# Kernel optimization log

Hardware: AMD Instinct MI355X
Metric: run time of the kernel (lower is better)

## Reference

```python
import math
import jax, jax.numpy as jnp
import numpy as np

R, C, D, ORDER = 2048, 2048, 64, 3
O = ORDER + 1  # var_size


def setup_inputs() -> dict:
    key = jax.random.key(0)
    k1, k2, k3, k4, k5, k6 = jax.random.split(key, 6)
    return {
        "events": jax.random.randint(k1, (R, C), 0, 2, dtype=jnp.int32),
        "col_times": jax.random.uniform(k2, (C,), dtype=jnp.float32),
        "z_rows": jax.random.normal(k3, (O, R, D), dtype=jnp.float32),
        "z_cols": jax.random.normal(k4, (C, D), dtype=jnp.float32),
        "gamma_rows": jax.random.uniform(k5, (R,), dtype=jnp.float32),
        "gamma_cols": jax.random.uniform(k6, (C,), dtype=jnp.float32),
    }


def reference(events, col_times, z_rows, z_cols, gamma_rows, gamma_cols):
    o = z_rows.shape[0]
    facts = np.array([math.factorial(i) for i in range(o)], dtype=np.float32)
    # Taylor time-basis: coeffs[o, c] = t_c^o / o!   (replaces nested Python loops)
    coeffs = jnp.stack([col_times ** i for i in range(o)]) / facts[:, None]  # (O, C)
    # row positions at each column's time: (R, C, D)
    pos = jnp.einsum('ord,oc->rcd', z_rows, coeffs)
    diff = pos - z_cols[None, :, :]                        # (R, C, D)
    dist = jnp.sqrt(jnp.sum(diff * diff, axis=-1))         # (R, C) pairwise L2
    logit = gamma_rows[:, None] + gamma_cols[None, :] - dist
    # log p where p = 1 - E - (1-2E)*sigmoid(logit):
    #   E==1 -> log sigmoid(logit); E==0 -> log sigmoid(-logit)
    sign = jnp.where(events == 1, 1.0, -1.0).astype(logit.dtype)
    log_lik = jnp.sum(jax.nn.log_sigmoid(sign * logit))
    return -log_lik
```

## Files before the change

### kernel.cpp

```cpp
#include <hip/hip_runtime.h>
#include <hip/hip_bf16.h>
#include <math.h>

#define R_DIM 2048
#define C_DIM 2048
#define D_DIM 64
#define K_TOT 288

typedef __attribute__((ext_vector_type(8))) short short8;
typedef __attribute__((ext_vector_type(4))) float floatx4;

__device__ __forceinline__ ushort f2bf(float f) {
  unsigned u = __float_as_uint(f);
  return (ushort)((u + 0x7FFFu + ((u >> 16) & 1u)) >> 16);
}

__global__ void prep_kernel(const int* __restrict__ events,
                            const float* __restrict__ col_times,
                            const float* __restrict__ z_rows,
                            const float* __restrict__ z_cols,
                            ushort* __restrict__ Ab,
                            ushort* __restrict__ Bb,
                            float* __restrict__ nzc,
                            unsigned char* __restrict__ Wb8,
                            float* __restrict__ out) {
  const int b = blockIdx.x;
  const int t = threadIdx.x;
  const int lane = t & 63;

  if (b == 0 && t == 0) out[0] = 0.0f;

  {
    const int4 e0 = *(const int4*)&events[(size_t)b * C_DIM + t * 8];
    const int4 e1 = *(const int4*)&events[(size_t)b * C_DIM + t * 8 + 4];
    const unsigned byte =
        (unsigned)(e0.x & 1) | ((unsigned)(e0.y & 1) << 1) |
        ((unsigned)(e0.z & 1) << 2) | ((unsigned)(e0.w & 1) << 3) |
        ((unsigned)(e1.x & 1) << 4) | ((unsigned)(e1.y & 1) << 5) |
        ((unsigned)(e1.z & 1) << 6) | ((unsigned)(e1.w & 1) << 7);
    Wb8[(size_t)b * 256 + t] = (unsigned char)byte;
  }

  if (t < 64) {
    float zv[4];
#pragma unroll
    for (int o = 0; o < 4; ++o) {
      zv[o] = z_rows[(size_t)(o * R_DIM + b) * D_DIM + lane];
      Ab[(size_t)b * K_TOT + o * 64 + lane] = f2bf(zv[o]);
    }
    float g00 = zv[0] * zv[0], g01 = zv[0] * zv[1], g02 = zv[0] * zv[2],
          g03 = zv[0] * zv[3], g11 = zv[1] * zv[1], g12 = zv[1] * zv[2],
          g13 = zv[1] * zv[3], g22 = zv[2] * zv[2], g23 = zv[2] * zv[3],
          g33 = zv[3] * zv[3];
#pragma unroll
    for (int off = 32; off > 0; off >>= 1) {
      g00 += __shfl_xor(g00, off); g01 += __shfl_xor(g01, off);
      g02 += __shfl_xor(g02, off); g03 += __shfl_xor(g03, off);
      g11 += __shfl_xor(g11, off); g12 += __shfl_xor(g12, off);
      g13 += __shfl_xor(g13, off); g22 += __shfl_xor(g22, off);
      g23 += __shfl_xor(g23, off); g33 += __shfl_xor(g33, off);
    }
    if (lane == 0) {
      ushort* e = Ab + (size_t)b * K_TOT + 256;
      e[0] = f2bf(g00);  e[1] = f2bf(g01);  e[2] = f2bf(g02);  e[3] = f2bf(g03);
      e[4] = f2bf(g01);  e[5] = f2bf(g11);  e[6] = f2bf(g12);  e[7] = f2bf(g13);
      e[8] = f2bf(g02);  e[9] = f2bf(g12);  e[10] = f2bf(g22); e[11] = f2bf(g23);
      e[12] = f2bf(g03); e[13] = f2bf(g13); e[14] = f2bf(g23); e[15] = f2bf(g33);
    }
    if (lane < 16) Ab[(size_t)b * K_TOT + 272 + lane] = 0;
  } else if (t < 128) {
    const float tt = col_times[b];
    float cf[4];
    cf[0] = 1.0f; cf[1] = tt; cf[2] = tt * tt * 0.5f;
    cf[3] = cf[2] * tt * (1.0f / 3.0f);
    const float zc = z_cols[(size_t)b * D_DIM + lane];
#pragma unroll
    for (int o = 0; o < 4; ++o)
      Bb[(size_t)b * K_TOT + o * 64 + lane] = f2bf(-2.0f * cf[o] * zc);
    float q = zc * zc;
#pragma unroll
    for (int off = 32; off > 0; off >>= 1) q += __shfl_xor(q, off);
    if (lane == 0) {
      nzc[b] = q;
      ushort* e = Bb + (size_t)b * K_TOT + 256;
#pragma unroll
      for (int i = 0; i < 16; ++i) e[i] = f2bf(cf[i >> 2] * cf[i & 3]);
    }
    if (lane < 16) Bb[(size_t)b * K_TOT + 272 + lane] = 0;
  }
}

__launch_bounds__(256, 4)
__global__ void pair_kernel(const float* __restrict__ gamma_rows,
                            const float* __restrict__ gamma_cols,
                            const ushort* __restrict__ Ab,
                            const ushort* __restrict__ Bb,
                            const float* __restrict__ nzc,
                            const unsigned char* __restrict__ Wb8,
                            float* __restrict__ out) {
  __shared__ float red[4];
  const int t = threadIdx.x;
  const int widx = t >> 6, lane = t & 63;
  const int m0 = blockIdx.y * 64, c0 = blockIdx.x * 64;
  const int wm = widx & 1, wn = widx >> 1;
  const int lm = lane & 15, kg = lane >> 4;

  const size_t wboff = (size_t)(c0 >> 3) + wn * 4;
  unsigned wbits[8];
  float grv[8];
#pragma unroll
  for (int mt = 0; mt < 2; ++mt)
#pragma unroll
    for (int j = 0; j < 4; ++j) {
      const int r = m0 + wm * 32 + mt * 16 + kg * 4 + j;
      wbits[mt * 4 + j] = *(const unsigned*)(Wb8 + (size_t)r * 256 + wboff);
      grv[mt * 4 + j] = gamma_rows[r];
    }
  float gcv[2], nzv[2];
#pragma unroll
  for (int nt = 0; nt < 2; ++nt) {
    const int c = c0 + wn * 32 + nt * 16 + lm;
    gcv[nt] = gamma_cols[c];
    nzv[nt] = nzc[c];
  }

  const ushort* a0p = Ab + (size_t)(m0 + wm * 32 + lm) * K_TOT + kg * 8;
  const ushort* a1p = a0p + 16 * K_TOT;
  const ushort* b0p = Bb + (size_t)(c0 + wn * 32 + lm) * K_TOT + kg * 8;
  const ushort* b1p = b0p + 16 * K_TOT;

  floatx4 acc[2][2];
#pragma unroll
  for (int i = 0; i < 2; ++i)
#pragma unroll
    for (int j = 0; j < 2; ++j) acc[i][j] = (floatx4){0.f, 0.f, 0.f, 0.f};

  short8 a0 = *(const short8*)(a0p);
  short8 a1 = *(const short8*)(a1p);
  short8 b0 = *(const short8*)(b0p);
  short8 b1 = *(const short8*)(b1p);
#pragma unroll
  for (int kt = 0; kt < 9; ++kt) {
    short8 na0, na1, nb0, nb1;
    if (kt < 8) {
      na0 = *(const short8*)(a0p + (kt + 1) * 32);
      na1 = *(const short8*)(a1p + (kt + 1) * 32);
      nb0 = *(const short8*)(b0p + (kt + 1) * 32);
      nb1 = *(const short8*)(b1p + (kt + 1) * 32);
    }
    acc[0][0] = __builtin_amdgcn_mfma_f32_16x16x32_bf16(a0, b0, acc[0][0], 0, 0, 0);
    acc[0][1] = __builtin_amdgcn_mfma_f32_16x16x32_bf16(a0, b1, acc[0][1], 0, 0, 0);
    acc[1][0] = __builtin_amdgcn_mfma_f32_16x16x32_bf16(a1, b0, acc[1][0], 0, 0, 0);
    acc[1][1] = __builtin_amdgcn_mfma_f32_16x16x32_bf16(a1, b1, acc[1][1], 0, 0, 0);
    if (kt == 2) {
      asm volatile("" ::"v"(wbits[0]), "v"(wbits[1]), "v"(wbits[2]),
                   "v"(wbits[3]), "v"(wbits[4]), "v"(wbits[5]), "v"(wbits[6]),
                   "v"(wbits[7]));
      asm volatile("" ::"v"(grv[0]), "v"(grv[1]), "v"(grv[2]), "v"(grv[3]),
                   "v"(grv[4]), "v"(grv[5]), "v"(grv[6]), "v"(grv[7]),
                   "v"(gcv[0]), "v"(gcv[1]), "v"(nzv[0]), "v"(nzv[1]));
    }
    a0 = na0; a1 = na1; b0 = nb0; b1 = nb1;
  }

  float lsum = 0.0f;
#pragma unroll
  for (int nt = 0; nt < 2; ++nt) {
    const int cbit = nt * 16 + lm;
#pragma unroll
    for (int mt = 0; mt < 2; ++mt) {
#pragma unroll
      for (int j = 0; j < 4; ++j) {
        const float evf = (float)((wbits[mt * 4 + j] >> cbit) & 1u);
        const float d2 = acc[mt][nt][j] + nzv[nt];
        const float dist = sqrtf(fmaxf(d2, 0.0f));
        const float logit = grv[mt * 4 + j] + gcv[nt] - dist;
        lsum += fmaxf(logit, 0.0f) + __logf(1.0f + __expf(-fabsf(logit))) -
                evf * logit;
      }
    }
  }
#pragma unroll
  for (int off = 32; off > 0; off >>= 1) lsum += __shfl_down(lsum, off);
  if (lane == 0) red[widx] = lsum;
  __syncthreads();
  if (t == 0) atomicAdd(out, red[0] + red[1] + red[2] + red[3]);
}

extern "C" void kernel_launch(void* const* d_in, const int* in_sizes, int n_in,
                              void* d_out, int out_size, void* d_ws, size_t ws_size,
                              hipStream_t stream) {
  const int* events = (const int*)d_in[0];
  const float* col_times = (const float*)d_in[1];
  const float* z_rows = (const float*)d_in[2];
  const float* z_cols = (const float*)d_in[3];
  const float* gamma_rows = (const float*)d_in[4];
  const float* gamma_cols = (const float*)d_in[5];
  float* out = (float*)d_out;

  ushort* Ab = (ushort*)d_ws;
  ushort* Bb = Ab + (size_t)R_DIM * K_TOT;
  float* nzc = (float*)(Bb + (size_t)C_DIM * K_TOT);
  unsigned char* Wb8 = (unsigned char*)(nzc + C_DIM);

  prep_kernel<<<R_DIM, 256, 0, stream>>>(events, col_times, z_rows, z_cols, Ab,
                                         Bb, nzc, Wb8, out);
  dim3 grid(C_DIM / 64, R_DIM / 64);
  pair_kernel<<<grid, 256, 0, stream>>>(gamma_rows, gamma_cols, Ab, Bb, nzc,
                                        Wb8, out);
}
```

Before: 95.30 us.

## Fuse bf16 operand packing and event reads into pair kernel, shrink prep

The prep kernel no longer packs the events bitmask or writes full bf16 copies of z_rows and the scaled z_cols. It now computes only the small Gram and Taylor-coefficient tails and the column norms. The pair kernel reads fp32 z_rows, z_cols and int32 events directly, scaling and converting to bf16 in registers before the MFMAs, plus one extra MFMA step for the 16-wide tail. This removes a large intermediate write and read, but each pair block now re-reads fp32 operands and int events, about twice the bytes, and does the conversion work redundantly across blocks. The output is zeroed with a memset instead of inside the prep kernel.

```diff
diff --git a/kernel.cpp b/kernel.cpp
--- a/kernel.cpp
+++ b/kernel.cpp
@@ -5,7 +5,6 @@
 #define R_DIM 2048
 #define C_DIM 2048
 #define D_DIM 64
-#define K_TOT 288
 
 typedef __attribute__((ext_vector_type(8))) short short8;
 typedef __attribute__((ext_vector_type(4))) float floatx4;
@@ -15,88 +14,73 @@
   return (ushort)((u + 0x7FFFu + ((u >> 16) & 1u)) >> 16);
 }
 
-__global__ void prep_kernel(const int* __restrict__ events,
+__device__ __forceinline__ short8 pack8(float4 a, float4 b) {
+  union { short8 s; __hip_bfloat162 h[4]; } u;
+  u.h[0] = __float22bfloat162_rn(make_float2(a.x, a.y));
+  u.h[1] = __float22bfloat162_rn(make_float2(a.z, a.w));
+  u.h[2] = __float22bfloat162_rn(make_float2(b.x, b.y));
+  u.h[3] = __float22bfloat162_rn(make_float2(b.z, b.w));
+  return u.s;
+}
+__device__ __forceinline__ float4 scale4(float s, float4 v) {
+  float4 r;
+  r.x = s * v.x; r.y = s * v.y; r.z = s * v.z; r.w = s * v.w;
+  return r;
+}
+
+__global__ void prep_kernel(const float* __restrict__ col_times,
+                            const float* __restrict__ z_rows,
+                            const float* __restrict__ z_cols,
+                            ushort* __restrict__ Ag,
+                            ushort* __restrict__ Bg,
+                            float* __restrict__ nzc) {
+  const int r = blockIdx.x;
+  const int lane = threadIdx.x;
+  float zv[4];
+#pragma unroll
+  for (int o = 0; o < 4; ++o)
+    zv[o] = z_rows[(size_t)(o * R_DIM + r) * D_DIM + lane];
+  float g00 = zv[0] * zv[0], g01 = zv[0] * zv[1], g02 = zv[0] * zv[2],
+        g03 = zv[0] * zv[3], g11 = zv[1] * zv[1], g12 = zv[1] * zv[2],
+        g13 = zv[1] * zv[3], g22 = zv[2] * zv[2], g23 = zv[2] * zv[3],
+        g33 = zv[3] * zv[3];
+#pragma unroll
+  for (int off = 32; off > 0; off >>= 1) {
+    g00 += __shfl_xor(g00, off); g01 += __shfl_xor(g01, off);
+    g02 += __shfl_xor(g02, off); g03 += __shfl_xor(g03, off);
+    g11 += __shfl_xor(g11, off); g12 += __shfl_xor(g12, off);
+    g13 += __shfl_xor(g13, off); g22 += __shfl_xor(g22, off);
+    g23 += __shfl_xor(g23, off); g33 += __shfl_xor(g33, off);
+  }
+  if (lane == 0) {
+    ushort* e = Ag + (size_t)r * 16;
+    e[0] = f2bf(g00);  e[1] = f2bf(g01);  e[2] = f2bf(g02);  e[3] = f2bf(g03);
+    e[4] = f2bf(g01);  e[5] = f2bf(g11);  e[6] = f2bf(g12);  e[7] = f2bf(g13);
+    e[8] = f2bf(g02);  e[9] = f2bf(g12);  e[10] = f2bf(g22); e[11] = f2bf(g23);
+    e[12] = f2bf(g03); e[13] = f2bf(g13); e[14] = f2bf(g23); e[15] = f2bf(g33);
+  }
+  const float zc = z_cols[(size_t)r * D_DIM + lane];
+  float q = zc * zc;
+#pragma unroll
+  for (int off = 32; off > 0; off >>= 1) q += __shfl_xor(q, off);
+  if (lane == 0) nzc[r] = q;
+  const float tt = col_times[r];
+  float cf[4];
+  cf[0] = 1.0f; cf[1] = tt; cf[2] = tt * tt * 0.5f;
+  cf[3] = cf[2] * tt * (1.0f / 3.0f);
+  if (lane < 16) Bg[(size_t)r * 16 + lane] = f2bf(cf[lane >> 2] * cf[lane & 3]);
+}
+
+__launch_bounds__(256, 4)
+__global__ void pair_kernel(const int* __restrict__ events,
                             const float* __restrict__ col_times,
                             const float* __restrict__ z_rows,
                             const float* __restrict__ z_cols,
-                            ushort* __restrict__ Ab,
-                            ushort* __restrict__ Bb,
-                            float* __restrict__ nzc,
-                            unsigned char* __restrict__ Wb8,
-                            float* __restrict__ out) {
-  const int b = blockIdx.x;
-  const int t = threadIdx.x;
-  const int lane = t & 63;
-
-  if (b == 0 && t == 0) out[0] = 0.0f;
-
-  {
-    const int4 e0 = *(const int4*)&events[(size_t)b * C_DIM + t * 8];
-    const int4 e1 = *(const int4*)&events[(size_t)b * C_DIM + t * 8 + 4];
-    const unsigned byte =
-        (unsigned)(e0.x & 1) | ((unsigned)(e0.y & 1) << 1) |
-        ((unsigned)(e0.z & 1) << 2) | ((unsigned)(e0.w & 1) << 3) |
-        ((unsigned)(e1.x & 1) << 4) | ((unsigned)(e1.y & 1) << 5) |
-        ((unsigned)(e1.z & 1) << 6) | ((unsigned)(e1.w & 1) << 7);
-    Wb8[(size_t)b * 256 + t] = (unsigned char)byte;
-  }
-
-  if (t < 64) {
-    float zv[4];
-#pragma unroll
-    for (int o = 0; o < 4; ++o) {
-      zv[o] = z_rows[(size_t)(o * R_DIM + b) * D_DIM + lane];
-      Ab[(size_t)b * K_TOT + o * 64 + lane] = f2bf(zv[o]);
-    }
-    float g00 = zv[0] * zv[0], g01 = zv[0] * zv[1], g02 = zv[0] * zv[2],
-          g03 = zv[0] * zv[3], g11 = zv[1] * zv[1], g12 = zv[1] * zv[2],
-          g13 = zv[1] * zv[3], g22 = zv[2] * zv[2], g23 = zv[2] * zv[3],
-          g33 = zv[3] * zv[3];
-#pragma unroll
-    for (int off = 32; off > 0; off >>= 1) {
-      g00 += __shfl_xor(g00, off); g01 += __shfl_xor(g01, off);
-      g02 += __shfl_xor(g02, off); g03 += __shfl_xor(g03, off);
-      g11 += __shfl_xor(g11, off); g12 += __shfl_xor(g12, off);
-      g13 += __shfl_xor(g13, off); g22 += __shfl_xor(g22, off);
-      g23 += __shfl_xor(g23, off); g33 += __shfl_xor(g33, off);
-    }
-    if (lane == 0) {
-      ushort* e = Ab + (size_t)b * K_TOT + 256;
-      e[0] = f2bf(g00);  e[1] = f2bf(g01);  e[2] = f2bf(g02);  e[3] = f2bf(g03);
-      e[4] = f2bf(g01);  e[5] = f2bf(g11);  e[6] = f2bf(g12);  e[7] = f2bf(g13);
-      e[8] = f2bf(g02);  e[9] = f2bf(g12);  e[10] = f2bf(g22); e[11] = f2bf(g23);
-      e[12] = f2bf(g03); e[13] = f2bf(g13); e[14] = f2bf(g23); e[15] = f2bf(g33);
-    }
-    if (lane < 16) Ab[(size_t)b * K_TOT + 272 + lane] = 0;
-  } else if (t < 128) {
-    const float tt = col_times[b];
-    float cf[4];
-    cf[0] = 1.0f; cf[1] = tt; cf[2] = tt * tt * 0.5f;
-    cf[3] = cf[2] * tt * (1.0f / 3.0f);
-    const float zc = z_cols[(size_t)b * D_DIM + lane];
-#pragma unroll
-    for (int o = 0; o < 4; ++o)
-      Bb[(size_t)b * K_TOT + o * 64 + lane] = f2bf(-2.0f * cf[o] * zc);
-    float q = zc * zc;
-#pragma unroll
-    for (int off = 32; off > 0; off >>= 1) q += __shfl_xor(q, off);
-    if (lane == 0) {
-      nzc[b] = q;
-      ushort* e = Bb + (size_t)b * K_TOT + 256;
-#pragma unroll
-      for (int i = 0; i < 16; ++i) e[i] = f2bf(cf[i >> 2] * cf[i & 3]);
-    }
-    if (lane < 16) Bb[(size_t)b * K_TOT + 272 + lane] = 0;
-  }
-}
-
-__launch_bounds__(256, 4)
-__global__ void pair_kernel(const float* __restrict__ gamma_rows,
+                            const float* __restrict__ gamma_rows,
                             const float* __restrict__ gamma_cols,
-                            const ushort* __restrict__ Ab,
-                            const ushort* __restrict__ Bb,
+                            const ushort* __restrict__ Ag,
+                            const ushort* __restrict__ Bg,
                             const float* __restrict__ nzc,
-                            const unsigned char* __restrict__ Wb8,
                             float* __restrict__ out) {
   __shared__ float red[4];
   const int t = threadIdx.x;
@@ -105,29 +89,32 @@
   const int wm = widx & 1, wn = widx >> 1;
   const int lm = lane & 15, kg = lane >> 4;
 
-  const size_t wboff = (size_t)(c0 >> 3) + wn * 4;
-  unsigned wbits[8];
+  int evv[16];
   float grv[8];
 #pragma unroll
   for (int mt = 0; mt < 2; ++mt)
 #pragma unroll
     for (int j = 0; j < 4; ++j) {
       const int r = m0 + wm * 32 + mt * 16 + kg * 4 + j;
-      wbits[mt * 4 + j] = *(const unsigned*)(Wb8 + (size_t)r * 256 + wboff);
       grv[mt * 4 + j] = gamma_rows[r];
-    }
-  float gcv[2], nzv[2];
+#pragma unroll
+      for (int nt = 0; nt < 2; ++nt)
+        evv[(mt * 4 + j) * 2 + nt] =
+            events[(size_t)r * C_DIM + c0 + wn * 32 + nt * 16 + lm];
+    }
+  float gcv[2], nzv[2], cf[2][4];
 #pragma unroll
   for (int nt = 0; nt < 2; ++nt) {
     const int c = c0 + wn * 32 + nt * 16 + lm;
     gcv[nt] = gamma_cols[c];
     nzv[nt] = nzc[c];
-  }
-
-  const ushort* a0p = Ab + (size_t)(m0 + wm * 32 + lm) * K_TOT + kg * 8;
-  const ushort* a1p = a0p + 16 * K_TOT;
-  const ushort* b0p = Bb + (size_t)(c0 + wn * 32 + lm) * K_TOT + kg * 8;
-  const ushort* b1p = b0p + 16 * K_TOT;
+    const float tt = col_times[c];
+    cf[nt][0] = 1.0f; cf[nt][1] = tt; cf[nt][2] = tt * tt * 0.5f;
+    cf[nt][3] = cf[nt][2] * tt * (1.0f / 3.0f);
+  }
+
+  const float* zra = z_rows + (size_t)(m0 + wm * 32 + lm) * D_DIM;
+  const float* zcb = z_cols + (size_t)(c0 + wn * 32 + lm) * D_DIM;
 
   floatx4 acc[2][2];
 #pragma unroll
@@ -135,43 +122,62 @@
 #pragma unroll
     for (int j = 0; j < 2; ++j) acc[i][j] = (floatx4){0.f, 0.f, 0.f, 0.f};
 
-  short8 a0 = *(const short8*)(a0p);
-  short8 a1 = *(const short8*)(a1p);
-  short8 b0 = *(const short8*)(b0p);
-  short8 b1 = *(const short8*)(b1p);
-#pragma unroll
-  for (int kt = 0; kt < 9; ++kt) {
-    short8 na0, na1, nb0, nb1;
-    if (kt < 8) {
-      na0 = *(const short8*)(a0p + (kt + 1) * 32);
-      na1 = *(const short8*)(a1p + (kt + 1) * 32);
-      nb0 = *(const short8*)(b0p + (kt + 1) * 32);
-      nb1 = *(const short8*)(b1p + (kt + 1) * 32);
-    }
-    acc[0][0] = __builtin_amdgcn_mfma_f32_16x16x32_bf16(a0, b0, acc[0][0], 0, 0, 0);
-    acc[0][1] = __builtin_amdgcn_mfma_f32_16x16x32_bf16(a0, b1, acc[0][1], 0, 0, 0);
-    acc[1][0] = __builtin_amdgcn_mfma_f32_16x16x32_bf16(a1, b0, acc[1][0], 0, 0, 0);
-    acc[1][1] = __builtin_amdgcn_mfma_f32_16x16x32_bf16(a1, b1, acc[1][1], 0, 0, 0);
+#pragma unroll
+  for (int kt = 0; kt < 8; ++kt) {
+    const int o = kt >> 1;
+    const int dk = (kt & 1) * 32 + kg * 8;
+    short8 af[2], bf[2];
+#pragma unroll
+    for (int mt = 0; mt < 2; ++mt) {
+      const float* p = zra + (size_t)o * R_DIM * D_DIM + mt * 16 * D_DIM + dk;
+      af[mt] = pack8(*(const float4*)p, *(const float4*)(p + 4));
+    }
+#pragma unroll
+    for (int nt = 0; nt < 2; ++nt) {
+      const float* p = zcb + nt * 16 * D_DIM + dk;
+      const float s = -2.0f * cf[nt][o];
+      bf[nt] = pack8(scale4(s, *(const float4*)p), scale4(s, *(const float4*)(p + 4)));
+    }
+    acc[0][0] = __builtin_amdgcn_mfma_f32_16x16x32_bf16(af[0], bf[0], acc[0][0], 0, 0, 0);
+    acc[0][1] = __builtin_amdgcn_mfma_f32_16x16x32_bf16(af[0], bf[1], acc[0][1], 0, 0, 0);
+    acc[1][0] = __builtin_amdgcn_mfma_f32_16x16x32_bf16(af[1], bf[0], acc[1][0], 0, 0, 0);
+    acc[1][1] = __builtin_amdgcn_mfma_f32_16x16x32_bf16(af[1], bf[1], acc[1][1], 0, 0, 0);
     if (kt == 2) {
-      asm volatile("" ::"v"(wbits[0]), "v"(wbits[1]), "v"(wbits[2]),
-                   "v"(wbits[3]), "v"(wbits[4]), "v"(wbits[5]), "v"(wbits[6]),
-                   "v"(wbits[7]));
+      asm volatile("" ::"v"(evv[0]), "v"(evv[1]), "v"(evv[2]), "v"(evv[3]),
+                   "v"(evv[4]), "v"(evv[5]), "v"(evv[6]), "v"(evv[7]));
+      asm volatile("" ::"v"(evv[8]), "v"(evv[9]), "v"(evv[10]), "v"(evv[11]),
+                   "v"(evv[12]), "v"(evv[13]), "v"(evv[14]), "v"(evv[15]));
       asm volatile("" ::"v"(grv[0]), "v"(grv[1]), "v"(grv[2]), "v"(grv[3]),
                    "v"(grv[4]), "v"(grv[5]), "v"(grv[6]), "v"(grv[7]),
                    "v"(gcv[0]), "v"(gcv[1]), "v"(nzv[0]), "v"(nzv[1]));
     }
-    a0 = na0; a1 = na1; b0 = nb0; b1 = nb1;
+  }
+  {
+    short8 af[2], bf[2];
+#pragma unroll
+    for (int mt = 0; mt < 2; ++mt)
+      af[mt] = (kg < 2)
+                   ? *(const short8*)(Ag + (size_t)(m0 + wm * 32 + mt * 16 + lm) * 16 + kg * 8)
+                   : (short8)0;
+#pragma unroll
+    for (int nt = 0; nt < 2; ++nt)
+      bf[nt] = (kg < 2)
+                   ? *(const short8*)(Bg + (size_t)(c0 + wn * 32 + nt * 16 + lm) * 16 + kg * 8)
+                   : (short8)0;
+    acc[0][0] = __builtin_amdgcn_mfma_f32_16x16x32_bf16(af[0], bf[0], acc[0][0], 0, 0, 0);
+    acc[0][1] = __builtin_amdgcn_mfma_f32_16x16x32_bf16(af[0], bf[1], acc[0][1], 0, 0, 0);
+    acc[1][0] = __builtin_amdgcn_mfma_f32_16x16x32_bf16(af[1], bf[0], acc[1][0], 0, 0, 0);
+    acc[1][1] = __builtin_amdgcn_mfma_f32_16x16x32_bf16(af[1], bf[1], acc[1][1], 0, 0, 0);
   }
 
   float lsum = 0.0f;
 #pragma unroll
   for (int nt = 0; nt < 2; ++nt) {
-    const int cbit = nt * 16 + lm;
 #pragma unroll
     for (int mt = 0; mt < 2; ++mt) {
 #pragma unroll
       for (int j = 0; j < 4; ++j) {
-        const float evf = (float)((wbits[mt * 4 + j] >> cbit) & 1u);
+        const float evf = (float)evv[(mt * 4 + j) * 2 + nt];
         const float d2 = acc[mt][nt][j] + nzv[nt];
         const float dist = sqrtf(fmaxf(d2, 0.0f));
         const float logit = grv[mt * 4 + j] + gcv[nt] - dist;
@@ -198,14 +204,14 @@
   const float* gamma_cols = (const float*)d_in[5];
   float* out = (float*)d_out;
 
-  ushort* Ab = (ushort*)d_ws;
-  ushort* Bb = Ab + (size_t)R_DIM * K_TOT;
-  float* nzc = (float*)(Bb + (size_t)C_DIM * K_TOT);
-  unsigned char* Wb8 = (unsigned char*)(nzc + C_DIM);
-
-  prep_kernel<<<R_DIM, 256, 0, stream>>>(events, col_times, z_rows, z_cols, Ab,
-                                         Bb, nzc, Wb8, out);
+  ushort* Ag = (ushort*)d_ws;
+  ushort* Bg = Ag + (size_t)R_DIM * 16;
+  float* nzc = (float*)(Bg + (size_t)C_DIM * 16);
+
+  hipMemsetAsync(d_out, 0, sizeof(float), stream);
+  prep_kernel<<<R_DIM, 64, 0, stream>>>(col_times, z_rows, z_cols, Ag, Bg, nzc);
   dim3 grid(C_DIM / 64, R_DIM / 64);
-  pair_kernel<<<grid, 256, 0, stream>>>(gamma_rows, gamma_cols, Ab, Bb, nzc,
-                                        Wb8, out);
-}
+  pair_kernel<<<grid, 256, 0, stream>>>(events, col_times, z_rows, z_cols,
+                                        gamma_rows, gamma_cols, Ag, Bg, nzc,
+                                        out);
+}
```

Result: slower. 108.2 us (+13.5%).

## Widen pair tiles to 64x128 and replace float atomics with last-block reduction

Applied to the files above, without the earlier changes.

Each pair block now covers 128 columns instead of 64, reusing the A fragments across two B column tiles, which halves the grid to 512 blocks and lowers the launch-bounds occupancy target. The final sum changes from one float atomicAdd per block to per-block partials plus a counter, and the last block to finish reduces them deterministically. This is meant to cut A-load traffic and atomic contention. In exchange it doubles accumulator registers and may reduce occupancy and tail parallelism.

```diff
diff --git a/kernel.cpp b/kernel.cpp
--- a/kernel.cpp
+++ b/kernel.cpp
@@ -6,6 +6,7 @@
 #define C_DIM 2048
 #define D_DIM 64
 #define K_TOT 288
+#define NBLK 512
 
 typedef __attribute__((ext_vector_type(8))) short short8;
 typedef __attribute__((ext_vector_type(4))) float floatx4;
@@ -23,12 +24,12 @@
                             ushort* __restrict__ Bb,
                             float* __restrict__ nzc,
                             unsigned char* __restrict__ Wb8,
-                            float* __restrict__ out) {
+                            unsigned* __restrict__ cnt) {
   const int b = blockIdx.x;
   const int t = threadIdx.x;
   const int lane = t & 63;
 
-  if (b == 0 && t == 0) out[0] = 0.0f;
+  if (b == 0 && t == 0) cnt[0] = 0u;
 
   {
     const int4 e0 = *(const int4*)&events[(size_t)b * C_DIM + t * 8];
@@ -90,101 +91,147 @@
   }
 }
 
-__launch_bounds__(256, 4)
+__launch_bounds__(256, 2)
 __global__ void pair_kernel(const float* __restrict__ gamma_rows,
                             const float* __restrict__ gamma_cols,
                             const ushort* __restrict__ Ab,
                             const ushort* __restrict__ Bb,
                             const float* __restrict__ nzc,
                             const unsigned char* __restrict__ Wb8,
+                            unsigned* __restrict__ cnt,
+                            float* __restrict__ parts,
                             float* __restrict__ out) {
   __shared__ float red[4];
+  __shared__ float flag;
   const int t = threadIdx.x;
   const int widx = t >> 6, lane = t & 63;
-  const int m0 = blockIdx.y * 64, c0 = blockIdx.x * 64;
+  const int m0 = blockIdx.y * 64, c0 = blockIdx.x * 128;
   const int wm = widx & 1, wn = widx >> 1;
   const int lm = lane & 15, kg = lane >> 4;
 
-  const size_t wboff = (size_t)(c0 >> 3) + wn * 4;
-  unsigned wbits[8];
+  unsigned wbits[2][8];
   float grv[8];
 #pragma unroll
   for (int mt = 0; mt < 2; ++mt)
 #pragma unroll
     for (int j = 0; j < 4; ++j) {
       const int r = m0 + wm * 32 + mt * 16 + kg * 4 + j;
-      wbits[mt * 4 + j] = *(const unsigned*)(Wb8 + (size_t)r * 256 + wboff);
       grv[mt * 4 + j] = gamma_rows[r];
-    }
-  float gcv[2], nzv[2];
-#pragma unroll
-  for (int nt = 0; nt < 2; ++nt) {
-    const int c = c0 + wn * 32 + nt * 16 + lm;
-    gcv[nt] = gamma_cols[c];
-    nzv[nt] = nzc[c];
-  }
+#pragma unroll
+      for (int ti = 0; ti < 2; ++ti)
+        wbits[ti][mt * 4 + j] = *(const unsigned*)(
+            Wb8 + (size_t)r * 256 + ((c0 + ti * 64) >> 3) + wn * 4);
+    }
+  float gcv[2][2], nzv[2][2];
+#pragma unroll
+  for (int ti = 0; ti < 2; ++ti)
+#pragma unroll
+    for (int nt = 0; nt < 2; ++nt) {
+      const int c = c0 + ti * 64 + wn * 32 + nt * 16 + lm;
+      gcv[ti][nt] = gamma_cols[c];
+      nzv[ti][nt] = nzc[c];
+    }
 
   const ushort* a0p = Ab + (size_t)(m0 + wm * 32 + lm) * K_TOT + kg * 8;
   const ushort* a1p = a0p + 16 * K_TOT;
-  const ushort* b0p = Bb + (size_t)(c0 + wn * 32 + lm) * K_TOT + kg * 8;
-  const ushort* b1p = b0p + 16 * K_TOT;
-
-  floatx4 acc[2][2];
-#pragma unroll
-  for (int i = 0; i < 2; ++i)
-#pragma unroll
-    for (int j = 0; j < 2; ++j) acc[i][j] = (floatx4){0.f, 0.f, 0.f, 0.f};
+  const ushort* bp[2][2];
+#pragma unroll
+  for (int ti = 0; ti < 2; ++ti) {
+    bp[ti][0] = Bb + (size_t)(c0 + ti * 64 + wn * 32 + lm) * K_TOT + kg * 8;
+    bp[ti][1] = bp[ti][0] + 16 * K_TOT;
+  }
+
+  floatx4 acc[2][2][2];
+#pragma unroll
+  for (int ti = 0; ti < 2; ++ti)
+#pragma unroll
+    for (int i = 0; i < 2; ++i)
+#pragma unroll
+      for (int j = 0; j < 2; ++j) acc[ti][i][j] = (floatx4){0.f, 0.f, 0.f, 0.f};
 
   short8 a0 = *(const short8*)(a0p);
   short8 a1 = *(const short8*)(a1p);
-  short8 b0 = *(const short8*)(b0p);
-  short8 b1 = *(const short8*)(b1p);
+  short8 b00 = *(const short8*)(bp[0][0]);
+  short8 b01 = *(const short8*)(bp[0][1]);
+  short8 b10 = *(const short8*)(bp[1][0]);
+  short8 b11 = *(const short8*)(bp[1][1]);
 #pragma unroll
   for (int kt = 0; kt < 9; ++kt) {
-    short8 na0, na1, nb0, nb1;
+    short8 na0, na1, nb00, nb01, nb10, nb11;
     if (kt < 8) {
       na0 = *(const short8*)(a0p + (kt + 1) * 32);
       na1 = *(const short8*)(a1p + (kt + 1) * 32);
-      nb0 = *(const short8*)(b0p + (kt + 1) * 32);
-      nb1 = *(const short8*)(b1p + (kt + 1) * 32);
-    }
-    acc[0][0] = __builtin_amdgcn_mfma_f32_16x16x32_bf16(a0, b0, acc[0][0], 0, 0, 0);
-    acc[0][1] = __builtin_amdgcn_mfma_f32_16x16x32_bf16(a0, b1, acc[0][1], 0, 0, 0);
-    acc[1][0] = __builtin_amdgcn_mfma_f32_16x16x32_bf16(a1, b0, acc[1][0], 0, 0, 0);
-    acc[1][1] = __builtin_amdgcn_mfma_f32_16x16x32_bf16(a1, b1, acc[1][1], 0, 0, 0);
+      nb00 = *(const short8*)(bp[0][0] + (kt + 1) * 32);
+      nb01 = *(const short8*)(bp[0][1] + (kt + 1) * 32);
+      nb10 = *(const short8*)(bp[1][0] + (kt + 1) * 32);
+      nb11 = *(const short8*)(bp[1][1] + (kt + 1) * 32);
+    }
+    acc[0][0][0] = __builtin_amdgcn_mfma_f32_16x16x32_bf16(a0, b00, acc[0][0][0], 0, 0, 0);
+    acc[0][0][1] = __builtin_amdgcn_mfma_f32_16x16x32_bf16(a0, b01, acc[0][0][1], 0, 0, 0);
+    acc[0][1][0] = __builtin_amdgcn_mfma_f32_16x16x32_bf16(a1, b00, acc[0][1][0], 0, 0, 0);
+    acc[0][1][1] = __builtin_amdgcn_mfma_f32_16x16x32_bf16(a1, b01, acc[0][1][1], 0, 0, 0);
+    acc[1][0][0] = __builtin_amdgcn_mfma_f32_16x16x32_bf16(a0, b10, acc[1][0][0], 0, 0, 0);
+    acc[1][0][1] = __builtin_amdgcn_mfma_f32_16x16x32_bf16(a0, b11, acc[1][0][1], 0, 0, 0);
+    acc[1][1][0] = __builtin_amdgcn_mfma_f32_16x16x32_bf16(a1, b10, acc[1][1][0], 0, 0, 0);
+    acc[1][1][1] = __builtin_amdgcn_mfma_f32_16x16x32_bf16(a1, b11, acc[1][1][1], 0, 0, 0);
     if (kt == 2) {
-      asm volatile("" ::"v"(wbits[0]), "v"(wbits[1]), "v"(wbits[2]),
-                   "v"(wbits[3]), "v"(wbits[4]), "v"(wbits[5]), "v"(wbits[6]),
-                   "v"(wbits[7]));
+      asm volatile("" ::"v"(wbits[0][0]), "v"(wbits[0][1]), "v"(wbits[0][2]),
+                   "v"(wbits[0][3]), "v"(wbits[0][4]), "v"(wbits[0][5]),
+                   "v"(wbits[0][6]), "v"(wbits[0][7]));
+      asm volatile("" ::"v"(wbits[1][0]), "v"(wbits[1][1]), "v"(wbits[1][2]),
+                   "v"(wbits[1][3]), "v"(wbits[1][4]), "v"(wbits[1][5]),
+                   "v"(wbits[1][6]), "v"(wbits[1][7]));
       asm volatile("" ::"v"(grv[0]), "v"(grv[1]), "v"(grv[2]), "v"(grv[3]),
-                   "v"(grv[4]), "v"(grv[5]), "v"(grv[6]), "v"(grv[7]),
-                   "v"(gcv[0]), "v"(gcv[1]), "v"(nzv[0]), "v"(nzv[1]));
-    }
-    a0 = na0; a1 = na1; b0 = nb0; b1 = nb1;
+                   "v"(grv[4]), "v"(grv[5]), "v"(grv[6]), "v"(grv[7]));
+      asm volatile("" ::"v"(gcv[0][0]), "v"(gcv[0][1]), "v"(gcv[1][0]),
+                   "v"(gcv[1][1]), "v"(nzv[0][0]), "v"(nzv[0][1]),
+                   "v"(nzv[1][0]), "v"(nzv[1][1]));
+    }
+    a0 = na0; a1 = na1; b00 = nb00; b01 = nb01; b10 = nb10; b11 = nb11;
   }
 
   float lsum = 0.0f;
 #pragma unroll
-  for (int nt = 0; nt < 2; ++nt) {
-    const int cbit = nt * 16 + lm;
-#pragma unroll
-    for (int mt = 0; mt < 2; ++mt) {
-#pragma unroll
-      for (int j = 0; j < 4; ++j) {
-        const float evf = (float)((wbits[mt * 4 + j] >> cbit) & 1u);
-        const float d2 = acc[mt][nt][j] + nzv[nt];
-        const float dist = sqrtf(fmaxf(d2, 0.0f));
-        const float logit = grv[mt * 4 + j] + gcv[nt] - dist;
-        lsum += fmaxf(logit, 0.0f) + __logf(1.0f + __expf(-fabsf(logit))) -
-                evf * logit;
+  for (int ti = 0; ti < 2; ++ti)
+#pragma unroll
+    for (int nt = 0; nt < 2; ++nt) {
+      const int cbit = nt * 16 + lm;
+#pragma unroll
+      for (int mt = 0; mt < 2; ++mt) {
+#pragma unroll
+        for (int j = 0; j < 4; ++j) {
+          const float evf = (float)((wbits[ti][mt * 4 + j] >> cbit) & 1u);
+          const float d2 = acc[ti][mt][nt][j] + nzv[ti][nt];
+          const float dist = sqrtf(fmaxf(d2, 0.0f));
+          const float logit = grv[mt * 4 + j] + gcv[ti][nt] - dist;
+          lsum += fmaxf(logit, 0.0f) + __logf(1.0f + __expf(-fabsf(logit))) -
+                  evf * logit;
+        }
       }
     }
-  }
 #pragma unroll
   for (int off = 32; off > 0; off >>= 1) lsum += __shfl_down(lsum, off);
   if (lane == 0) red[widx] = lsum;
   __syncthreads();
-  if (t == 0) atomicAdd(out, red[0] + red[1] + red[2] + red[3]);
+
+  const int bid = blockIdx.y * gridDim.x + blockIdx.x;
+  if (t == 0) {
+    parts[bid] = red[0] + red[1] + red[2] + red[3];
+    __threadfence();
+    const unsigned old = atomicAdd(cnt, 1u);
+    flag = (old == NBLK - 1) ? 1.0f : 0.0f;
+  }
+  __syncthreads();
+  if (flag != 0.0f) {
+    __threadfence();
+    float s = 0.0f;
+    for (int i = t; i < NBLK; i += 256) s += atomicAdd(&parts[i], 0.0f);
+#pragma unroll
+    for (int off = 32; off > 0; off >>= 1) s += __shfl_down(s, off);
+    if (lane == 0) red[widx] = s;
+    __syncthreads();
+    if (t == 0) out[0] = red[0] + red[1] + red[2] + red[3];
+  }
 }
 
 extern "C" void kernel_launch(void* const* d_in, const int* in_sizes, int n_in,
@@ -202,10 +249,12 @@
   ushort* Bb = Ab + (size_t)R_DIM * K_TOT;
   float* nzc = (float*)(Bb + (size_t)C_DIM * K_TOT);
   unsigned char* Wb8 = (unsigned char*)(nzc + C_DIM);
+  unsigned* cnt = (unsigned*)(Wb8 + (size_t)R_DIM * 256);
+  float* parts = (float*)(cnt + 16);
 
   prep_kernel<<<R_DIM, 256, 0, stream>>>(events, col_times, z_rows, z_cols, Ab,
-                                         Bb, nzc, Wb8, out);
-  dim3 grid(C_DIM / 64, R_DIM / 64);
+                                         Bb, nzc, Wb8, cnt);
+  dim3 grid(16, 32);
   pair_kernel<<<grid, 256, 0, stream>>>(gamma_rows, gamma_cols, Ab, Bb, nzc,
-                                        Wb8, out);
-}
+                                        Wb8, cnt, parts, out);
+}
```

After: 97.90 us. +2.7%, slower.
